# Optimization experiments

Measured on AMD Instinct MI355X. Metric: run time of the kernel, lower is better.

The kernel has to match this reference:

```python
import jax, jax.numpy as jnp
import numpy as np

EMBED_DIM = 1024
NUM_HEADS = 16
SEQ_LEN = 2048
BATCH = 2
LN_EPS = 1e-5


def setup_inputs() -> dict:
    key = jax.random.key(0)
    ks = jax.random.split(key, 12)
    d = EMBED_DIM
    s = 1.0 / np.sqrt(d)
    inp = {
        "x": jax.random.normal(ks[0], (BATCH, SEQ_LEN, d), dtype=jnp.float32),
        "ln1_g": jnp.ones((d,), jnp.float32),
        "ln1_b": jnp.zeros((d,), jnp.float32),
        "ln2_g": jnp.ones((d,), jnp.float32),
        "ln2_b": jnp.zeros((d,), jnp.float32),
        "W_qkv": jax.random.normal(ks[1], (d, 3 * d), jnp.float32) * s,
        "b_qkv": jnp.zeros((3 * d,), jnp.float32),
        "W_proj": jax.random.normal(ks[2], (d, d), jnp.float32) * s,
        "b_proj": jnp.zeros((d,), jnp.float32),
        "W_fc": jax.random.normal(ks[3], (d, 4 * d), jnp.float32) * s,
        "b_fc": jnp.zeros((4 * d,), jnp.float32),
        "W_out": jax.random.normal(ks[4], (4 * d, d), jnpp_dummy := jnp.float32) * (1.0 / np.sqrt(4 * d)),
        "b_out": jnp.zeros((d,), jnp.float32),
    }
    return inp


def _layernorm(x, g, b):
    mu = jnp.mean(x, axis=-1, keepdims=True)
    var = jnp.mean(jnp.square(x - mu), axis=-1, keepdims=True)
    return (x - mu) * jax.lax.rsqrt(var + LN_EPS) * g + b


def _block(x, ln1_g, ln1_b, ln2_g, ln2_b, W_qkv, b_qkv, W_proj, b_proj, W_fc, b_fc, W_out, b_out):
    B, S, D = x.shape
    H = NUM_HEADS
    hd = D // H
    h = _layernorm(x, ln1_g, ln1_b)
    qkv = h @ W_qkv + b_qkv  # [B,S,3D]
    q, k, v = jnp.split(qkv, 3, axis=-1)
    # [B,H,S,hd]
    q = q.reshape(B, S, H, hd).transpose(0, 2, 1, 3)
    k = k.reshape(B, S, H, hd).transpose(0, 2, 1, 3)
    v = v.reshape(B, S, H, hd).transpose(0, 2, 1, 3)
    attn = jnp.einsum("bhqd,bhkd->bhqk", q, k) / np.sqrt(hd).astype(np.float32)
    causal = jnp.tril(jnp.ones((S, S), dtype=bool))
    attn = jnp.where(causal, attn, -jnp.inf)
    attn = jax.nn.softmax(attn, axis=-1)
    y = jnp.einsum("bhqk,bhkd->bhqd", attn, v)
    y = y.transpose(0, 2, 1, 3).reshape(B, S, D)
    y = y @ W_proj + b_proj
    x = x + y
    h2 = _layernorm(x, ln2_g, ln2_b)
    m = jax.nn.relu(h2 @ W_fc + b_fc) @ W_out + b_out
    return x + m


def reference(x, ln1_g, ln1_b, ln2_g, ln2_b, W_qkv, b_qkv, W_proj, b_proj, W_fc, b_fc, W_out, b_out):
    return _block(x, ln1_g, ln1_b, ln2_g, ln2_b, W_qkv, b_qkv, W_proj, b_proj, W_fc, b_fc, W_out, b_out)
```

## Files before the change

kernel.cpp:

```cpp
#include <hip/hip_runtime.h>

typedef unsigned short u16;
typedef __attribute__((ext_vector_type(8))) __bf16 bf16x8;
typedef __attribute__((ext_vector_type(4))) float f32x4;

#define DEV __device__ __forceinline__

DEV u16 f2bf(float f) {
  unsigned u = __float_as_uint(f);
  u += 0x7fffu + ((u >> 16) & 1u);
  return (u16)(u >> 16);
}
DEV float bf2f(u16 u) { return __uint_as_float((unsigned)u << 16); }

DEV void gl_lds16(const void* g, void* l) {
  __builtin_amdgcn_global_load_lds(
      (const __attribute__((address_space(1))) void*)(uintptr_t)g,
      (__attribute__((address_space(3))) void*)(unsigned)(uintptr_t)l, 16, 0, 0);
}

DEV float wave_sum64(float v) {
#pragma unroll
  for (int off = 32; off > 0; off >>= 1) v += __shfl_down(v, off);
  return v;
}

DEV void ln_body(const float4 v, const float* g, const float* be, u16* out_row, int t,
                 float* red) {
  const int w = t >> 6, L = t & 63;
  float s = v.x + v.y + v.z + v.w;
  s = wave_sum64(s);
  if (L == 0) red[w] = s;
  __syncthreads();
  const float mean = (red[0] + red[1] + red[2] + red[3]) * (1.0f / 1024.0f);
  const float dx = v.x - mean, dy = v.y - mean, dz = v.z - mean, dw = v.w - mean;
  float q = dx * dx + dy * dy + dz * dz + dw * dw;
  q = wave_sum64(q);
  if (L == 0) red[4 + w] = q;
  __syncthreads();
  const float var = (red[4] + red[5] + red[6] + red[7]) * (1.0f / 1024.0f);
  const float rs = rsqrtf(var + 1e-5f);
  const float4 gg = reinterpret_cast<const float4*>(g)[t];
  const float4 bb = reinterpret_cast<const float4*>(be)[t];
  ushort4 o;
  o.x = f2bf(dx * rs * gg.x + bb.x);
  o.y = f2bf(dy * rs * gg.y + bb.y);
  o.z = f2bf(dz * rs * gg.z + bb.z);
  o.w = f2bf(dw * rs * gg.w + bb.w);
  reinterpret_cast<ushort4*>(out_row)[t] = o;
}

__global__ __launch_bounds__(256) void prep_kernel(
    const float* __restrict__ x, const float* __restrict__ ln1g,
    const float* __restrict__ ln1b, u16* __restrict__ hbuf,
    const float* __restrict__ Wqkv, u16* __restrict__ wt_qkv,
    const float* __restrict__ Wproj, u16* __restrict__ wt_proj,
    const float* __restrict__ Wfc, u16* __restrict__ wt_fc,
    const float* __restrict__ Wout, u16* __restrict__ wt_out) {
  __shared__ float smem[32 * 33];
  int id = blockIdx.x;
  const int t = threadIdx.x;
  if (id < 4096) {
    const float4 v = reinterpret_cast<const float4*>(x + (size_t)id * 1024)[t];
    ln_body(v, ln1g, ln1b, hbuf + (size_t)id * 1024, t, smem);
    return;
  }
  id -= 4096;
  const float* W;
  u16* Wt;
  int K, N, nbx;
  if (id < 3072) {
    W = Wqkv; Wt = wt_qkv; K = 1024; N = 3072; nbx = 96;
  } else if (id < 3072 + 1024) {
    id -= 3072; W = Wproj; Wt = wt_proj; K = 1024; N = 1024; nbx = 32;
  } else if (id < 3072 + 1024 + 4096) {
    id -= 3072 + 1024; W = Wfc; Wt = wt_fc; K = 1024; N = 4096; nbx = 128;
  } else {
    id -= 3072 + 1024 + 4096; W = Wout; Wt = wt_out; K = 4096; N = 1024; nbx = 32;
  }
  float(*tile)[33] = (float(*)[33])smem;
  const int c0 = (id % nbx) * 32, r0 = (id / nbx) * 32;
  const int tx = t & 31, ty = t >> 5;
#pragma unroll
  for (int j = 0; j < 4; ++j)
    tile[ty + j * 8][tx] = W[(size_t)(r0 + ty + j * 8) * N + c0 + tx];
  __syncthreads();
#pragma unroll
  for (int j = 0; j < 4; ++j) {
    const int n = c0 + ty + j * 8, k = r0 + tx;
    Wt[(size_t)n * K + k] = f2bf(tile[tx][ty + j * 8]);
  }
}

__global__ __launch_bounds__(256) void proj_reduce_ln(const float* __restrict__ x,
                                                      const float* __restrict__ bias,
                                                      const u16* __restrict__ P0,
                                                      const u16* __restrict__ P1,
                                                      const float* __restrict__ g,
                                                      const float* __restrict__ be,
                                                      float* __restrict__ x2,
                                                      u16* __restrict__ hbuf) {
  const int row = blockIdx.x, t = threadIdx.x;
  const size_t off = (size_t)row * 1024;
  __shared__ float red[8];
  const float4 xv = reinterpret_cast<const float4*>(x + off)[t];
  const float4 bv = reinterpret_cast<const float4*>(bias)[t];
  const ushort4 p0 = reinterpret_cast<const ushort4*>(P0 + off)[t];
  const ushort4 p1 = reinterpret_cast<const ushort4*>(P1 + off)[t];
  float4 v;
  v.x = xv.x + bv.x + bf2f(p0.x) + bf2f(p1.x);
  v.y = xv.y + bv.y + bf2f(p0.y) + bf2f(p1.y);
  v.z = xv.z + bv.z + bf2f(p0.z) + bf2f(p1.z);
  v.w = xv.w + bv.w + bf2f(p0.w) + bf2f(p1.w);
  reinterpret_cast<float4*>(x2 + off)[t] = v;
  ln_body(v, g, be, hbuf + off, t, red);
}

__global__ __launch_bounds__(256) void out_reduce(const float* __restrict__ x2,
                                                  const float* __restrict__ bias,
                                                  const u16* __restrict__ P0,
                                                  const u16* __restrict__ P1,
                                                  const u16* __restrict__ P2,
                                                  const u16* __restrict__ P3,
                                                  float* __restrict__ dout) {
  const int row = blockIdx.x, t = threadIdx.x;
  const size_t off = (size_t)row * 1024;
  const float4 xv = reinterpret_cast<const float4*>(x2 + off)[t];
  const float4 bv = reinterpret_cast<const float4*>(bias)[t];
  const ushort4 a = reinterpret_cast<const ushort4*>(P0 + off)[t];
  const ushort4 b = reinterpret_cast<const ushort4*>(P1 + off)[t];
  const ushort4 c = reinterpret_cast<const ushort4*>(P2 + off)[t];
  const ushort4 d = reinterpret_cast<const ushort4*>(P3 + off)[t];
  float4 o;
  o.x = xv.x + bv.x + bf2f(a.x) + bf2f(b.x) + bf2f(c.x) + bf2f(d.x);
  o.y = xv.y + bv.y + bf2f(a.y) + bf2f(b.y) + bf2f(c.y) + bf2f(d.y);
  o.z = xv.z + bv.z + bf2f(a.z) + bf2f(b.z) + bf2f(c.z) + bf2f(d.z);
  o.w = xv.w + bv.w + bf2f(a.w) + bf2f(b.w) + bf2f(c.w) + bf2f(d.w);
  reinterpret_cast<float4*>(dout + off)[t] = o;
}

enum { F_BIAS = 1, F_RESID = 2, F_RELU = 4, F_BF16 = 8, F_PART4 = 32, F_VT = 64 };

template <int FLAGS>
__global__ __launch_bounds__(256, 2) void gemm_bt(const u16* __restrict__ A,
                                                  const u16* __restrict__ Bt,
                                                  const float* __restrict__ bias,
                                                  const float* __restrict__ resid,
                                                  void* __restrict__ Cout,
                                                  u16* __restrict__ pp0, u16* __restrict__ pp1,
                                                  u16* __restrict__ pp2, u16* __restrict__ pp3,
                                                  int M, int N, int K, int Kst) {
  __shared__ __attribute__((aligned(16))) u16 sA[2][128 * 32];
  __shared__ __attribute__((aligned(16))) u16 sB[2][128 * 32];

  const int gx = gridDim.x, gy = gridDim.y;
  const int tilesPerZ = gx * gy;
  int lin = (blockIdx.z * gy + blockIdx.y) * gx + blockIdx.x;
  const int total = tilesPerZ * gridDim.z;
  if (!(total & 7)) lin = (lin & 7) * (total >> 3) + (lin >> 3);
  const int zz = lin / tilesPerZ;
  const int pid = lin - zz * tilesPerZ;
  const int npg = gx << 3;
  const int gid = pid / npg;
  const int rem = pid - gid * npg;
  const int fm = gid << 3;
  const int gsm = (gy - fm < 8) ? (gy - fm) : 8;
  const int bm = fm + rem % gsm;
  const int bn = rem / gsm;

  const int t = threadIdx.x, w = t >> 6, L = t & 63, quad = L >> 4, l15 = L & 15;
  const int wm = w >> 1, wn = w & 1;
  const int m0 = bm * 128, n0 = bn * 128;
  const u16* Ag = A + (size_t)m0 * Kst + (size_t)zz * K;
  const u16* Bg = Bt + (size_t)n0 * Kst + (size_t)zz * K;

  f32x4 acc[4][4] = {};

  for (int k0 = 0; k0 < K; k0 += 64) {
    __syncthreads();
#pragma unroll
    for (int h = 0; h < 2; ++h) {
#pragma unroll
      for (int i = 0; i < 2; ++i) {
        const int cp = i * 256 + t, rr = cp >> 2, cc = (cp & 3) << 3;
        gl_lds16(Ag + (size_t)rr * Kst + k0 + h * 32 + cc, &sA[h][(i * 256 + w * 64) * 8]);
      }
#pragma unroll
      for (int i = 0; i < 2; ++i) {
        const int cp = i * 256 + t, rr = cp >> 2, cc = (cp & 3) << 3;
        gl_lds16(Bg + (size_t)rr * Kst + k0 + h * 32 + cc, &sB[h][(i * 256 + w * 64) * 8]);
      }
    }
    __syncthreads();

#pragma unroll
    for (int h = 0; h < 2; ++h) {
      bf16x8 af[4], bfr[4];
#pragma unroll
      for (int m = 0; m < 4; ++m)
        af[m] = *(const bf16x8*)&sA[h][(wm * 64 + m * 16 + l15) * 32 + quad * 8];
#pragma unroll
      for (int n = 0; n < 4; ++n)
        bfr[n] = *(const bf16x8*)&sB[h][(wn * 64 + n * 16 + l15) * 32 + quad * 8];
#pragma unroll
      for (int m = 0; m < 4; ++m)
#pragma unroll
        for (int n = 0; n < 4; ++n)
          acc[m][n] =
              __builtin_amdgcn_mfma_f32_16x16x32_bf16(af[m], bfr[n], acc[m][n], 0, 0, 0);
    }
  }

  if ((FLAGS & F_VT) && n0 >= 2048) {
#pragma unroll
    for (int m = 0; m < 4; ++m) {
#pragma unroll
      for (int n = 0; n < 4; ++n) {
        const int col = n0 + wn * 64 + n * 16 + l15;
        const float bv = bias[col];
        const int hh = (col - 2048) >> 6, dd = col & 63;
        const int srow = m0 + wm * 64 + m * 16 + quad * 4;
        const int bb = srow >> 11, ss = srow & 2047;
        ushort4 tmp;
        tmp.x = f2bf(acc[m][n][0] + bv);
        tmp.y = f2bf(acc[m][n][1] + bv);
        tmp.z = f2bf(acc[m][n][2] + bv);
        tmp.w = f2bf(acc[m][n][3] + bv);
        *(ushort4*)(pp0 + ((size_t)((bb * 16 + hh) * 64 + dd)) * 2048 + ss) = tmp;
      }
    }
    return;
  }

  u16* pbase = nullptr;
  if (FLAGS & F_PART4)
    pbase = (zz == 0) ? pp0 : (zz == 1) ? pp1 : (zz == 2) ? pp2 : pp3;

#pragma unroll
  for (int m = 0; m < 4; ++m) {
#pragma unroll
    for (int n = 0; n < 4; ++n) {
      const int col = n0 + wn * 64 + n * 16 + l15;
      const float bv = (FLAGS & F_BIAS) ? bias[col] : 0.0f;
#pragma unroll
      for (int rr = 0; rr < 4; ++rr) {
        const int row = m0 + wm * 64 + m * 16 + quad * 4 + rr;
        if (FLAGS & F_PART4) {
          pbase[(size_t)row * N + col] = f2bf(acc[m][n][rr]);
        } else {
          float v = acc[m][n][rr] + bv;
          if (FLAGS & F_RESID) v += resid[(size_t)row * N + col];
          if (FLAGS & F_RELU) v = fmaxf(v, 0.0f);
          if (FLAGS & F_BF16)
            ((u16*)Cout)[(size_t)row * N + col] = f2bf(v);
          else
            ((float*)Cout)[(size_t)row * N + col] = v;
        }
      }
    }
  }
}

__global__ __launch_bounds__(256) void flash_attn(const u16* __restrict__ qkv,
                                                  const u16* __restrict__ Vt,
                                                  u16* __restrict__ y) {
  constexpr int S = 2048, D3 = 3072, D = 1024;
  constexpr float Csc = 0.125f * 1.44269504088896f;
  __shared__ __attribute__((aligned(16))) u16 sK[2][64 * 64];
  __shared__ __attribute__((aligned(16))) u16 sV[2][64 * 64];
  __shared__ __attribute__((aligned(16))) u16 sP[4][2 * 16 * 40];

  const int lin = blockIdx.x;
  const int half = lin >> 9, rem = lin & 511;
  const int qt = half ? (31 - (rem & 31)) : (rem & 31);
  const int bh = (rem >> 5) | (half << 4);
  const int b = bh >> 4, h = bh & 15;
  const int q0 = qt * 64;

  const int t = threadIdx.x, w = t >> 6, L = t & 63, quad = L >> 4, l15 = L & 15;
  const int qw = q0 + w * 16;

  const u16* qbase = qkv + (size_t)(b * S) * D3 + h * 64;
  const u16* Kbase = qbase + D;
  const u16* Vbase = Vt + (size_t)((b * 16 + h) * 64) * S;

  const u16* Ksrc[2];
  const u16* Vsrc[2];
#pragma unroll
  for (int i = 0; i < 2; ++i) {
    const int p = i * 256 + t;
    const int row = p >> 3;
    const int k8 = ((p & 7) ^ (row & 7)) << 3;
    Ksrc[i] = Kbase + (size_t)row * D3 + k8;
    Vsrc[i] = Vbase + (size_t)row * S + k8;
  }

  bf16x8 aQ[2];
#pragma unroll
  for (int kk = 0; kk < 2; ++kk)
    aQ[kk] = *(const bf16x8*)(qbase + (size_t)(qw + l15) * D3 + kk * 32 + quad * 8);

  bf16x8 ones;
#pragma unroll
  for (int i = 0; i < 8; ++i) ones[i] = (__bf16)1.0f;

  f32x4 acc[4] = {};
  f32x4 lacc = {};

  u16* sPw = sP[w];
  const int swz = l15 & 7;
  const int nkv = qt + 1;

#pragma unroll
  for (int i = 0; i < 2; ++i)
    gl_lds16(Ksrc[i], &sK[0][(i * 256 + w * 64) * 8]);
#pragma unroll
  for (int i = 0; i < 2; ++i)
    gl_lds16(Vsrc[i], &sV[0][(i * 256 + w * 64) * 8]);

  int cur = 0;
  for (int it = 0; it < nkv; ++it) {
    const int kv0 = it * 64;
    if (it + 1 < nkv) {
      const int kvn = kv0 + 64;
#pragma unroll
      for (int i = 0; i < 2; ++i)
        gl_lds16(Ksrc[i] + (size_t)kvn * D3, &sK[cur ^ 1][(i * 256 + w * 64) * 8]);
#pragma unroll
      for (int i = 0; i < 2; ++i)
        gl_lds16(Vsrc[i] + kvn, &sV[cur ^ 1][(i * 256 + w * 64) * 8]);
      asm volatile("s_waitcnt vmcnt(4)" ::: "memory");
    } else {
      asm volatile("s_waitcnt vmcnt(0)" ::: "memory");
    }
    __builtin_amdgcn_s_barrier();

    const u16* sKc = sK[cur];
    const u16* sVc = sV[cur];

    f32x4 s[4] = {};
#pragma unroll
    for (int kk = 0; kk < 2; ++kk) {
#pragma unroll
      for (int n = 0; n < 4; ++n) {
        const bf16x8 bK =
            *(const bf16x8*)&sKc[(n * 16 + l15) * 64 + ((kk * 4 + quad) ^ swz) * 8];
        s[n] = __builtin_amdgcn_mfma_f32_16x16x32_bf16(aQ[kk], bK, s[n], 0, 0, 0);
      }
    }

    if (kv0 + 63 > qw) {
#pragma unroll
      for (int n = 0; n < 4; ++n) {
        const int col = kv0 + n * 16 + l15;
#pragma unroll
        for (int r = 0; r < 4; ++r) {
          const int row = qw + quad * 4 + r;
          const float p = __builtin_amdgcn_exp2f(s[n][r] * Csc);
          s[n][r] = (col > row) ? 0.0f : p;
        }
      }
    } else {
#pragma unroll
      for (int n = 0; n < 4; ++n)
#pragma unroll
        for (int r = 0; r < 4; ++r) s[n][r] = __builtin_amdgcn_exp2f(s[n][r] * Csc);
    }

#pragma unroll
    for (int n = 0; n < 4; ++n)
#pragma unroll
      for (int r = 0; r < 4; ++r)
        sPw[(n >> 1) * 640 + (quad * 4 + r) * 40 + (n & 1) * 16 + l15] = f2bf(s[n][r]);

#pragma unroll
    for (int kk = 0; kk < 2; ++kk) {
      const bf16x8 aP = *(const bf16x8*)&sPw[kk * 640 + l15 * 40 + quad * 8];
      lacc = __builtin_amdgcn_mfma_f32_16x16x32_bf16(aP, ones, lacc, 0, 0, 0);
#pragma unroll
      for (int dn = 0; dn < 4; ++dn) {
        const bf16x8 bV =
            *(const bf16x8*)&sVc[(dn * 16 + l15) * 64 + ((kk * 4 + quad) ^ swz) * 8];
        acc[dn] = __builtin_amdgcn_mfma_f32_16x16x32_bf16(aP, bV, acc[dn], 0, 0, 0);
      }
    }

    asm volatile("s_waitcnt lgkmcnt(0)" ::: "memory");
    __builtin_amdgcn_s_barrier();
    cur ^= 1;
  }

#pragma unroll
  for (int r = 0; r < 4; ++r) {
    const float inv = 1.0f / lacc[r];
    const int row = qw + quad * 4 + r;
    u16* yb = y + (size_t)(b * S + row) * D + h * 64 + l15;
#pragma unroll
    for (int dn = 0; dn < 4; ++dn) yb[dn * 16] = f2bf(acc[dn][r] * inv);
  }
}

extern "C" void kernel_launch(void* const* d_in, const int* in_sizes, int n_in,
                              void* d_out, int out_size, void* d_ws, size_t ws_size,
                              hipStream_t stream) {
  const float* x = (const float*)d_in[0];
  const float* ln1g = (const float*)d_in[1];
  const float* ln1b = (const float*)d_in[2];
  const float* ln2g = (const float*)d_in[3];
  const float* ln2b = (const float*)d_in[4];
  const float* Wqkv = (const float*)d_in[5];
  const float* bqkv = (const float*)d_in[6];
  const float* Wproj = (const float*)d_in[7];
  const float* bproj = (const float*)d_in[8];
  const float* Wfc = (const float*)d_in[9];
  const float* bfc = (const float*)d_in[10];
  const float* Wout = (const float*)d_in[11];
  const float* bout = (const float*)d_in[12];

  char* ws = (char*)d_ws;
  const size_t MB = 1u << 20;
  u16* wt_out = (u16*)(ws + 0 * MB);
  u16* hbuf = (u16*)(ws + 8 * MB);
  float* x2 = (float*)(ws + 16 * MB);
  u16* ybuf = (u16*)(ws + 32 * MB);
  u16* qkvb = (u16*)(ws + 40 * MB);
  u16* vtb = (u16*)(ws + 64 * MB);
  u16* wt_qkv = (u16*)(ws + 72 * MB);
  u16* wt_proj = (u16*)(ws + 78 * MB);
  u16* wt_fc = (u16*)(ws + 80 * MB);
  u16* projP0 = (u16*)(ws + 40 * MB);
  u16* projP1 = (u16*)(ws + 48 * MB);
  u16* m1 = (u16*)(ws + 40 * MB);
  u16* po0 = (u16*)(ws + 8 * MB);
  u16* po1 = (u16*)(ws + 32 * MB);
  u16* po2 = (u16*)(ws + 72 * MB);
  u16* po3 = (u16*)(ws + 80 * MB);

  prep_kernel<<<4096 + 3072 + 1024 + 4096 + 4096, 256, 0, stream>>>(
      x, ln1g, ln1b, hbuf, Wqkv, wt_qkv, Wproj, wt_proj, Wfc, wt_fc, Wout, wt_out);

  gemm_bt<F_BIAS | F_BF16 | F_VT><<<dim3(24, 32), 256, 0, stream>>>(
      hbuf, wt_qkv, bqkv, nullptr, qkvb, vtb, nullptr, nullptr, nullptr,
      4096, 3072, 1024, 1024);
  flash_attn<<<1024, 256, 0, stream>>>(qkvb, vtb, ybuf);

  gemm_bt<F_PART4><<<dim3(8, 32, 2), 256, 0, stream>>>(
      ybuf, wt_proj, nullptr, nullptr, nullptr, projP0, projP1, nullptr, nullptr,
      4096, 1024, 512, 1024);
  proj_reduce_ln<<<4096, 256, 0, stream>>>(x, bproj, projP0, projP1, ln2g, ln2b, x2, hbuf);

  gemm_bt<F_BIAS | F_RELU | F_BF16><<<dim3(32, 32), 256, 0, stream>>>(
      hbuf, wt_fc, bfc, nullptr, m1, nullptr, nullptr, nullptr, nullptr,
      4096, 4096, 1024, 1024);

  gemm_bt<F_PART4><<<dim3(8, 32, 4), 256, 0, stream>>>(
      m1, wt_out, nullptr, nullptr, nullptr, po0, po1, po2, po3,
      4096, 1024, 1024, 4096);
  out_reduce<<<4096, 256, 0, stream>>>(x2, bout, po0, po1, po2, po3, (float*)d_out);
}
```

Baseline: 323.9 us.

## Split long causal query tiles across KV halves and combine partials

Flash attention now splits each query tile in the upper half of the sequence into two KV-range parts: one covering KV tiles 0-15 and one covering tiles 16 through the diagonal. Each part writes unnormalized fp32 accumulators and row sums, and a new combine kernel adds them and normalizes. Lower-half tiles still run in one pass. This raises the block count from 1024 to 1536 to balance the uneven causal work. The K/V LDS double buffer is also replaced by a single buffer with the prefetch issued after the barrier, which cuts LDS use but removes the load/compute overlap. It adds an extra launch and fp32 partial traffic through the workspace.

```diff
diff --git a/kernel.cpp b/kernel.cpp
--- a/kernel.cpp
+++ b/kernel.cpp
@@ -263,17 +263,31 @@
 
 __global__ __launch_bounds__(256) void flash_attn(const u16* __restrict__ qkv,
                                                   const u16* __restrict__ Vt,
-                                                  u16* __restrict__ y) {
+                                                  u16* __restrict__ y,
+                                                  float* __restrict__ acc0,
+                                                  float* __restrict__ acc1,
+                                                  float* __restrict__ lacc0,
+                                                  float* __restrict__ lacc1) {
   constexpr int S = 2048, D3 = 3072, D = 1024;
   constexpr float Csc = 0.125f * 1.44269504088896f;
-  __shared__ __attribute__((aligned(16))) u16 sK[2][64 * 64];
-  __shared__ __attribute__((aligned(16))) u16 sV[2][64 * 64];
+  __shared__ __attribute__((aligned(16))) u16 sK[64 * 64];
+  __shared__ __attribute__((aligned(16))) u16 sV[64 * 64];
   __shared__ __attribute__((aligned(16))) u16 sP[4][2 * 16 * 40];
 
-  const int lin = blockIdx.x;
-  const int half = lin >> 9, rem = lin & 511;
-  const int qt = half ? (31 - (rem & 31)) : (rem & 31);
-  const int bh = (rem >> 5) | (half << 4);
+  const int bid = blockIdx.x;
+  const int bh = bid & 31;
+  const int e = bid >> 5;
+  int qt, it0, it1, part;
+  if (e < 16) {
+    qt = 16 + e; it0 = 0; it1 = 16; part = 1;
+  } else {
+    const int j = (e - 16) >> 1;
+    if (((e - 16) & 1) == 0) {
+      qt = 15 - j; it0 = 0; it1 = qt + 1; part = 0;
+    } else {
+      qt = 31 - j; it0 = 16; it1 = qt + 1; part = 2;
+    }
+  }
   const int b = bh >> 4, h = bh & 15;
   const int q0 = qt * 64;
 
@@ -309,34 +323,21 @@
 
   u16* sPw = sP[w];
   const int swz = l15 & 7;
-  const int nkv = qt + 1;
-
-#pragma unroll
-  for (int i = 0; i < 2; ++i)
-    gl_lds16(Ksrc[i], &sK[0][(i * 256 + w * 64) * 8]);
-#pragma unroll
-  for (int i = 0; i < 2; ++i)
-    gl_lds16(Vsrc[i], &sV[0][(i * 256 + w * 64) * 8]);
-
-  int cur = 0;
-  for (int it = 0; it < nkv; ++it) {
+
+  {
+    const int kv0 = it0 * 64;
+#pragma unroll
+    for (int i = 0; i < 2; ++i)
+      gl_lds16(Ksrc[i] + (size_t)kv0 * D3, &sK[(i * 256 + w * 64) * 8]);
+#pragma unroll
+    for (int i = 0; i < 2; ++i)
+      gl_lds16(Vsrc[i] + kv0, &sV[(i * 256 + w * 64) * 8]);
+  }
+
+  for (int it = it0; it < it1; ++it) {
     const int kv0 = it * 64;
-    if (it + 1 < nkv) {
-      const int kvn = kv0 + 64;
-#pragma unroll
-      for (int i = 0; i < 2; ++i)
-        gl_lds16(Ksrc[i] + (size_t)kvn * D3, &sK[cur ^ 1][(i * 256 + w * 64) * 8]);
-#pragma unroll
-      for (int i = 0; i < 2; ++i)
-        gl_lds16(Vsrc[i] + kvn, &sV[cur ^ 1][(i * 256 + w * 64) * 8]);
-      asm volatile("s_waitcnt vmcnt(4)" ::: "memory");
-    } else {
-      asm volatile("s_waitcnt vmcnt(0)" ::: "memory");
-    }
+    asm volatile("s_waitcnt vmcnt(0)" ::: "memory");
     __builtin_amdgcn_s_barrier();
-
-    const u16* sKc = sK[cur];
-    const u16* sVc = sV[cur];
 
     f32x4 s[4] = {};
 #pragma unroll
@@ -344,7 +345,7 @@
 #pragma unroll
       for (int n = 0; n < 4; ++n) {
         const bf16x8 bK =
-            *(const bf16x8*)&sKc[(n * 16 + l15) * 64 + ((kk * 4 + quad) ^ swz) * 8];
+            *(const bf16x8*)&sK[(n * 16 + l15) * 64 + ((kk * 4 + quad) ^ swz) * 8];
         s[n] = __builtin_amdgcn_mfma_f32_16x16x32_bf16(aQ[kk], bK, s[n], 0, 0, 0);
       }
     }
@@ -380,24 +381,63 @@
 #pragma unroll
       for (int dn = 0; dn < 4; ++dn) {
         const bf16x8 bV =
-            *(const bf16x8*)&sVc[(dn * 16 + l15) * 64 + ((kk * 4 + quad) ^ swz) * 8];
+            *(const bf16x8*)&sV[(dn * 16 + l15) * 64 + ((kk * 4 + quad) ^ swz) * 8];
         acc[dn] = __builtin_amdgcn_mfma_f32_16x16x32_bf16(aP, bV, acc[dn], 0, 0, 0);
       }
     }
 
     asm volatile("s_waitcnt lgkmcnt(0)" ::: "memory");
     __builtin_amdgcn_s_barrier();
-    cur ^= 1;
-  }
-
-#pragma unroll
-  for (int r = 0; r < 4; ++r) {
-    const float inv = 1.0f / lacc[r];
-    const int row = qw + quad * 4 + r;
-    u16* yb = y + (size_t)(b * S + row) * D + h * 64 + l15;
-#pragma unroll
-    for (int dn = 0; dn < 4; ++dn) yb[dn * 16] = f2bf(acc[dn][r] * inv);
-  }
+    if (it + 1 < it1) {
+      const int kvn = kv0 + 64;
+#pragma unroll
+      for (int i = 0; i < 2; ++i)
+        gl_lds16(Ksrc[i] + (size_t)kvn * D3, &sK[(i * 256 + w * 64) * 8]);
+#pragma unroll
+      for (int i = 0; i < 2; ++i)
+        gl_lds16(Vsrc[i] + kvn, &sV[(i * 256 + w * 64) * 8]);
+    }
+  }
+
+  if (part == 0) {
+#pragma unroll
+    for (int r = 0; r < 4; ++r) {
+      const float inv = 1.0f / lacc[r];
+      const int row = qw + quad * 4 + r;
+      u16* yb = y + (size_t)(b * S + row) * D + h * 64 + l15;
+#pragma unroll
+      for (int dn = 0; dn < 4; ++dn) yb[dn * 16] = f2bf(acc[dn][r] * inv);
+    }
+  } else {
+    float* accP = (part == 1) ? acc0 : acc1;
+    float* laccP = (part == 1) ? lacc0 : lacc1;
+#pragma unroll
+    for (int r = 0; r < 4; ++r) {
+      const int row = qw + quad * 4 + r;
+      const int g = (bh << 10) + (row - 1024);
+      float* ap = accP + (size_t)g * 64 + l15;
+#pragma unroll
+      for (int dn = 0; dn < 4; ++dn) ap[dn * 16] = acc[dn][r];
+      if (l15 == 0) laccP[g] = lacc[r];
+    }
+  }
+}
+
+__global__ __launch_bounds__(256) void attn_combine(const float* __restrict__ acc0,
+                                                    const float* __restrict__ acc1,
+                                                    const float* __restrict__ lacc0,
+                                                    const float* __restrict__ lacc1,
+                                                    u16* __restrict__ y) {
+  const int t = threadIdx.x;
+  const int g = blockIdx.x * 4 + (t >> 6);
+  const int d = t & 63;
+  const int bh = g >> 10, ri = g & 1023;
+  const int b = bh >> 4, h = bh & 15;
+  const int row = 1024 + ri;
+  const size_t po = (size_t)g * 64 + d;
+  const float l = lacc0[g] + lacc1[g];
+  const float v = (acc0[po] + acc1[po]) / l;
+  y[((size_t)(b * 2048 + row)) * 1024 + h * 64 + d] = f2bf(v);
 }
 
 extern "C" void kernel_launch(void* const* d_in, const int* in_sizes, int n_in,
@@ -435,6 +475,10 @@
   u16* po1 = (u16*)(ws + 32 * MB);
   u16* po2 = (u16*)(ws + 72 * MB);
   u16* po3 = (u16*)(ws + 80 * MB);
+  float* facc0 = (float*)(ws + 8 * MB);
+  float* facc1 = (float*)(ws + 16 * MB);
+  float* flacc0 = (float*)(ws + 24 * MB);
+  float* flacc1 = (float*)(ws + 25 * MB);
 
   prep_kernel<<<4096 + 3072 + 1024 + 4096 + 4096, 256, 0, stream>>>(
       x, ln1g, ln1b, hbuf, Wqkv, wt_qkv, Wproj, wt_proj, Wfc, wt_fc, Wout, wt_out);
@@ -442,7 +486,8 @@
   gemm_bt<F_BIAS | F_BF16 | F_VT><<<dim3(24, 32), 256, 0, stream>>>(
       hbuf, wt_qkv, bqkv, nullptr, qkvb, vtb, nullptr, nullptr, nullptr,
       4096, 3072, 1024, 1024);
-  flash_attn<<<1024, 256, 0, stream>>>(qkvb, vtb, ybuf);
+  flash_attn<<<1536, 256, 0, stream>>>(qkvb, vtb, ybuf, facc0, facc1, flacc0, flacc1);
+  attn_combine<<<8192, 256, 0, stream>>>(facc0, facc1, flacc0, flacc1, ybuf);
 
   gemm_bt<F_PART4><<<dim3(8, 32, 2), 256, 0, stream>>>(
       ybuf, wt_proj, nullptr, nullptr, nullptr, projP0, projP1, nullptr, nullptr,
```

After: 319.7 us. No clear change (-1.3%).
